# Kernel optimization log

Measured on AMD Instinct MI355X. Metric: run time of the kernel, lower is better.

## Reference

```python
import jax, jax.numpy as jnp
import numpy as np
from jax import lax

N_SERIES = 1024   # embedding rows
B = 1024          # batch (= rows of Y)
T = 512           # n_time
INPUT = 28        # input_size
OUTPUT = 28       # output_size
N_T = 2           # temporal exogenous channels
N_S = 4           # static features
M = 7             # seasonality[0]


def setup_inputs() -> dict:
    key = jax.random.key(0)
    k1, k2, k3, k4, k5 = jax.random.split(key, 5)
    S = jax.random.normal(k1, (B, N_S), jnp.float32)
    # Y must be strictly positive (division + log in normalize)
    Y = jax.random.uniform(k2, (B, T), jnp.float32, 0.5, 1.5)
    X = jax.random.normal(k3, (B, N_T, T), jnp.float32)
    idxs = jax.random.randint(k4, (B,), 0, N_SERIES)
    sample_mask = jnp.ones((B, T), jnp.float32)
    # embedding table, init near 0.5 like the torch module
    embeds_weight = 0.5 + 0.05 * jax.random.normal(k5, (N_SERIES, 1 + 1 + M), jnp.float32)
    return dict(S=S, Y=Y, X=X, idxs=idxs, sample_mask=sample_mask,
                embeds_weight=embeds_weight)


def _levels_seasons(Y, embeds):
    """Single-seasonality (len(seasonality)==1) ES recurrence via lax.scan."""
    lev_sms = jax.nn.sigmoid(embeds[:, 0])      # [B]
    seas_sms = jax.nn.sigmoid(embeds[:, 1])     # [B]
    init_seas = jnp.exp(embeds[:, 2:2 + M])     # [B, M]
    s0 = init_seas[:, 0]                        # [B]
    lev0 = Y[:, 0] / s0                         # levels[0] = Y0 / seas_prod
    # seasonalities1 list = [s0..s_{M-1}, s0]; step t uses index t, so the
    # rolling buffer of the next M seasonal values starts as [s1..s_{M-1}, s0]
    buf0 = jnp.concatenate([init_seas[:, 1:], s0[:, None]], axis=1)  # [B, M]

    def step(carry, y_t):
        lev, buf = carry
        seas_t = buf[:, 0]
        newlev = lev_sms * (y_t / seas_t) + (1.0 - lev_sms) * lev
        newseas = seas_sms * (y_t / newlev) + (1.0 - seas_sms) * seas_t
        buf = jnp.concatenate([buf[:, 1:], newseas[:, None]], axis=1)
        return (newlev, buf), (newlev, newseas)

    (_, _), (levs, seass) = lax.scan(step, (lev0, buf0), Y[:, 1:].T)  # [T-1, B]
    levels = jnp.concatenate([lev0[:, None], levs.T], axis=1)         # [B, T]
    init_list = jnp.concatenate([init_seas, s0[:, None]], axis=1)     # [B, M+1]
    seasonalities = jnp.concatenate([init_list, seass.T], axis=1)     # [B, T+M]
    return levels, seasonalities


def _forward_core(S, Y, X, idxs, sample_mask, embeds_weight):
    embeds = embeds_weight[idxs]                    # embedding lookup [B, 9]
    levels, seasonalities = _levels_seasons(Y, embeds)

    W = T - INPUT - OUTPUT + 1                      # n_windows
    starts = jnp.arange(W)
    idx_in = starts[:, None] + jnp.arange(INPUT)    # [W, INPUT]

    Yw = Y[:, idx_in]                               # [B, W, INPUT]
    lev_end = levels[:, starts + INPUT - 1]         # [B, W] level at window end
    seas_in = seasonalities[:, idx_in]              # [B, W, INPUT]
    insample = jnp.log(Yw / (lev_end[:, :, None] * seas_in))  # [B, W, INPUT]

    # temporal exogenous: X[:, :, start:end+OUTPUT].reshape(B, -1)
    idx_x = starts[:, None] + jnp.arange(INPUT + OUTPUT)       # [W, I+O]
    Xw = X[:, :, idx_x]                              # [B, N_T, W, I+O]
    Xw = jnp.transpose(Xw, (0, 2, 1, 3)).reshape(Y.shape[0], W, N_T * (INPUT + OUTPUT))
    insample = jnp.concatenate([insample, Xw], axis=2)

    # static features
    Sw = jnp.broadcast_to(S[:, None, :], (Y.shape[0], W, N_S))
    insample = jnp.concatenate([insample, Sw], axis=2)          # [B, W, C]
    windows_y_insample = jnp.transpose(insample, (1, 0, 2))     # [W, B, C]

    # outsample (eval mode: raw Y, not normalized)
    idx_out = starts[:, None] + INPUT + jnp.arange(OUTPUT)      # [W, OUTPUT]
    windows_y_outsample = jnp.transpose(Y[:, idx_out], (1, 0, 2))  # [W, B, O]

    # sample_mask unfold(size=OUTPUT, step=1), keep last W windows
    n_unf = T - OUTPUT + 1
    starts_m = jnp.arange(n_unf)[-W:]
    idx_m = starts_m[:, None] + jnp.arange(OUTPUT)
    mask_w = jnp.transpose(sample_mask[:, idx_m], (1, 0, 2))    # [W, B, O]

    return windows_y_insample, windows_y_outsample, levels, seasonalities, mask_w


def reference(S, Y, X, idxs, sample_mask, embeds_weight):
    return _forward_core(S, Y, X, idxs, sample_mask, embeds_weight)
```

## Files before the change

### kernel.cpp

```cpp
#include <hip/hip_runtime.h>

#define BB   1024
#define TT   512
#define NIN  28
#define NOUT 28
#define NS   4
#define MM   7
#define WW   457
#define SLEN 519
#define EMB  9

#define OUT1_SZ (WW * BB * 144)
#define OUT2_SZ (WW * BB * 28)
#define OUT3_SZ (BB * TT)
#define OUT4_SZ (BB * SLEN)

#define CH   32
#define NCH  (TT / CH)

typedef float f4 __attribute__((ext_vector_type(4)));

__device__ __forceinline__ f4 ld4u(const float* p) {
    f4 v;
    __builtin_memcpy(&v, p, sizeof(f4));
    return v;
}

__global__ __launch_bounds__(64) void es_scan(const float* __restrict__ Y,
        const int* __restrict__ idxs, const float* __restrict__ EW,
        float* __restrict__ levels, float* __restrict__ seas) {
    __shared__ float yl[64][CH + 1];
    __shared__ float se[64][CH + 1];
    const int tid = threadIdx.x;
    const int b0  = blockIdx.x << 6;
    const int b   = b0 + tid;

    const float* e = EW + idxs[b] * EMB;
    const float lev_sms  = 1.0f / (1.0f + __expf(-e[0]));
    const float seas_sms = 1.0f / (1.0f + __expf(-e[1]));
    const float a_l = 1.0f - lev_sms;
    const float a_s = 1.0f - seas_sms;

    float buf[MM];
    const float is0 = __expf(e[2]);
    {
        float* srow = seas + b * SLEN;
        srow[0] = is0;
#pragma unroll
        for (int k = 1; k < MM; ++k) {
            float v = __expf(e[2 + k]);
            srow[k] = v;
            buf[k - 1] = v;
        }
        buf[MM - 1] = is0;
    }

    f4 pf[8];
#pragma unroll
    for (int k = 0; k < 8; ++k) {
        int flat = (k << 6) + tid;
        int r = flat >> 3, q = flat & 7;
        pf[k] = *reinterpret_cast<const f4*>(Y + (b0 + r) * TT + (q << 2));
    }

    float lev = 0.0f;

#define ES_STEP(TTI)                                                        \
    {                                                                       \
        float y  = yreg[TTI];                                               \
        float st = buf[0];                                                  \
        lev = lev_sms * __fdividef(y, st) + a_l * lev;                      \
        float ns = seas_sms * __fdividef(y, lev) + a_s * st;                \
        buf[0] = buf[1]; buf[1] = buf[2]; buf[2] = buf[3];                  \
        buf[3] = buf[4]; buf[4] = buf[5]; buf[5] = buf[6];                  \
        buf[6] = ns;                                                        \
        yl[tid][TTI] = lev;                                                 \
        se[tid][TTI] = ns;                                                  \
    }

    for (int c = 0; c < NCH; ++c) {
        __syncthreads();
#pragma unroll
        for (int k = 0; k < 8; ++k) {
            int flat = (k << 6) + tid;
            int r = flat >> 3, q = flat & 7;
            float* dst = &yl[r][q << 2];
            dst[0] = pf[k].x; dst[1] = pf[k].y; dst[2] = pf[k].z; dst[3] = pf[k].w;
        }
        __syncthreads();
        if (c < NCH - 1) {
#pragma unroll
            for (int k = 0; k < 8; ++k) {
                int flat = (k << 6) + tid;
                int r = flat >> 3, q = flat & 7;
                pf[k] = *reinterpret_cast<const f4*>(
                    Y + (b0 + r) * TT + (c + 1) * CH + (q << 2));
            }
        }

        float yreg[CH];
#pragma unroll
        for (int tt = 0; tt < CH; ++tt) yreg[tt] = yl[tid][tt];

        if (c == 0) {
            lev = __fdividef(yreg[0], is0);
            yl[tid][0] = lev;
            se[tid][0] = is0;
#pragma unroll
            for (int tt = 1; tt < CH; ++tt) ES_STEP(tt)
        } else {
#pragma unroll
            for (int tt = 0; tt < CH; ++tt) ES_STEP(tt)
        }
        __syncthreads();

#pragma unroll
        for (int k = 0; k < CH; ++k) {
            int flat = (k << 6) + tid;
            int r    = flat >> 5;
            int col  = flat & 31;
            levels[(b0 + r) * TT   + c * CH + col]      = yl[r][col];
            seas  [(b0 + r) * SLEN + MM + c * CH + col] = se[r][col];
        }
    }
#undef ES_STEP
}

#define PD 129

__global__ __launch_bounds__(256) void k_out1(const float* __restrict__ S,
        const float* __restrict__ Y, const float* __restrict__ X,
        const float* __restrict__ levels, const float* __restrict__ seas,
        f4* __restrict__ out1) {
    __shared__ f4    Xr[4 * 2 * 2 * PD];
    __shared__ f4    LYSr[4 * 2 * PD];
    __shared__ float LL[2][512];
    __shared__ float LYSp[2][520];

    const int tid = threadIdx.x;
    const int b0  = blockIdx.x << 1;

    for (int u = tid; u < 1024; u += 256) {
        int bl = u >> 9, t = u & 511;
        int b  = b0 + bl;
        LL[bl][t]   = __logf(levels[b * TT + t]);
        LYSp[bl][t] = __logf(Y[b * TT + t]) - __logf(seas[b * SLEN + t]);
    }
    __syncthreads();

    for (int u = tid; u < 1024; u += 256) {
        int s = u >> 8, r = u & 255, bl = r >> 7, k = r & 127;
        int base = 4 * k + s;
        f4 v;
        v.x = LYSp[bl][base];     v.y = LYSp[bl][base + 1];
        v.z = LYSp[bl][base + 2]; v.w = LYSp[bl][base + 3];
        LYSr[(s * 2 + bl) * PD + k] = v;
    }
    for (int u = tid; u < 2048; u += 256) {
        int s = u >> 9, r = u & 511, bl = r >> 8, ch = (r >> 7) & 1, k = r & 127;
        int start = 4 * k + s; if (start > 508) start = 508;
        Xr[((s * 2 + bl) * 2 + ch) * PD + k] =
            ld4u(X + (size_t)((b0 + bl) * 2 + ch) * TT + start);
    }
    f4 Sv0 = *reinterpret_cast<const f4*>(S + b0 * NS);
    f4 Sv1 = *reinterpret_cast<const f4*>(S + (b0 + 1) * NS);
    __syncthreads();

    for (int j = tid; j < WW * 72; j += 256) {
        int g   = j / 72;
        int r   = j - g * 72;
        int bl  = (r >= 36) ? 1 : 0;
        int col = r - 36 * bl;
        int s   = g & 3;
        int whi = g >> 2;
        f4 v;
        if (col < 7) {
            f4 t = LYSr[(s * 2 + bl) * PD + whi + col];
            float ll = LL[bl][g + 27];
            v.x = t.x - ll; v.y = t.y - ll; v.z = t.z - ll; v.w = t.w - ll;
        } else if (col < 35) {
            int ch = (col >= 21) ? 1 : 0;
            int jj = col - 7 - 14 * ch;
            v = Xr[((s * 2 + bl) * 2 + ch) * PD + whi + jj];
        } else {
            v = bl ? Sv1 : Sv0;
        }
        __builtin_nontemporal_store(v, &out1[((g << 10) + b0 + bl) * 36 + col]);
    }
}

#define NF2 (WW * BB * 7)

__global__ __launch_bounds__(256) void k_out25(const float* __restrict__ Y,
        const float* __restrict__ mask, f4* __restrict__ out2,
        f4* __restrict__ out5) {
    int i = blockIdx.x * blockDim.x + threadIdx.x;
    const int stride = gridDim.x * blockDim.x;
    for (; i < NF2; i += stride) {
        int wb = i / 7;
        int j  = i - wb * 7;
        int b  = wb & (BB - 1);
        int w  = wb >> 10;
        int base = w + NIN + (j << 2);
        f4 vy = ld4u(Y    + b * TT + base);
        f4 vm = ld4u(mask + b * TT + base);
        __builtin_nontemporal_store(vy, &out2[i]);
        __builtin_nontemporal_store(vm, &out5[i]);
    }
}

extern "C" void kernel_launch(void* const* d_in, const int* in_sizes, int n_in,
                              void* d_out, int out_size, void* d_ws, size_t ws_size,
                              hipStream_t stream) {
    const float* S    = (const float*)d_in[0];
    const float* Y    = (const float*)d_in[1];
    const float* X    = (const float*)d_in[2];
    const int*   idxs = (const int*)d_in[3];
    const float* mask = (const float*)d_in[4];
    const float* EW   = (const float*)d_in[5];

    float* out  = (float*)d_out;
    float* out1 = out;
    float* out2 = out1 + OUT1_SZ;
    float* out3 = out2 + OUT2_SZ;
    float* out4 = out3 + OUT3_SZ;
    float* out5 = out4 + OUT4_SZ;

    es_scan<<<16, 64, 0, stream>>>(Y, idxs, EW, out3, out4);
    k_out1<<<BB / 2, 256, 0, stream>>>(S, Y, X, out3, out4, (f4*)out1);
    k_out25<<<2048, 256, 0, stream>>>(Y, mask, (f4*)out2, (f4*)out5);
}
```

Baseline: 130.0 us.

## Fuse ES scan with out2/out5 copy kernel and split out1 across more blocks

The serial ES scan (16 blocks) now shares one launch with the out2/out5 gather copy, so the copy blocks fill the GPU while the scan runs instead of waiting behind it. The scan blocks grow to 256 threads, with only 64 doing the recurrence and all helping with loads and stores. k_out1 is split four ways along the window dimension (2048 blocks) and reads unrotated shared arrays with scalar LDS loads instead of the pre-rotated f4 layout. Each k_out1 block still recomputes the logs for its full rows, which repeats transcendental work four times.

```diff
diff --git a/kernel.cpp b/kernel.cpp
--- a/kernel.cpp
+++ b/kernel.cpp
@@ -17,6 +17,7 @@
 
 #define CH   32
 #define NCH  (TT / CH)
+#define NF2  (WW * BB * 7)
 
 typedef float f4 __attribute__((ext_vector_type(4)));
 
@@ -26,44 +27,49 @@
     return v;
 }
 
-__global__ __launch_bounds__(64) void es_scan(const float* __restrict__ Y,
-        const int* __restrict__ idxs, const float* __restrict__ EW,
-        float* __restrict__ levels, float* __restrict__ seas) {
+__global__ __launch_bounds__(256, 8) void k_scan_out25(
+        const float* __restrict__ Y, const int* __restrict__ idxs,
+        const float* __restrict__ EW, const float* __restrict__ mask,
+        float* __restrict__ levels, float* __restrict__ seas,
+        f4* __restrict__ out2, f4* __restrict__ out5) {
     __shared__ float yl[64][CH + 1];
     __shared__ float se[64][CH + 1];
+
     const int tid = threadIdx.x;
-    const int b0  = blockIdx.x << 6;
-    const int b   = b0 + tid;
-
-    const float* e = EW + idxs[b] * EMB;
-    const float lev_sms  = 1.0f / (1.0f + __expf(-e[0]));
-    const float seas_sms = 1.0f / (1.0f + __expf(-e[1]));
-    const float a_l = 1.0f - lev_sms;
-    const float a_s = 1.0f - seas_sms;
-
-    float buf[MM];
-    const float is0 = __expf(e[2]);
-    {
-        float* srow = seas + b * SLEN;
-        srow[0] = is0;
-#pragma unroll
-        for (int k = 1; k < MM; ++k) {
-            float v = __expf(e[2 + k]);
-            srow[k] = v;
-            buf[k - 1] = v;
-        }
-        buf[MM - 1] = is0;
-    }
-
-    f4 pf[8];
-#pragma unroll
-    for (int k = 0; k < 8; ++k) {
-        int flat = (k << 6) + tid;
-        int r = flat >> 3, q = flat & 7;
-        pf[k] = *reinterpret_cast<const f4*>(Y + (b0 + r) * TT + (q << 2));
-    }
-
-    float lev = 0.0f;
+
+    if (blockIdx.x < 16) {
+        const int b0 = blockIdx.x << 6;
+        const int bs = b0 + (tid & 63);
+
+        const float* e = EW + idxs[bs] * EMB;
+        const float lev_sms  = 1.0f / (1.0f + __expf(-e[0]));
+        const float seas_sms = 1.0f / (1.0f + __expf(-e[1]));
+        const float a_l = 1.0f - lev_sms;
+        const float a_s = 1.0f - seas_sms;
+
+        float buf[MM];
+        const float is0 = __expf(e[2]);
+        {
+            float* srow = seas + bs * SLEN;
+            if (tid < 64) srow[0] = is0;
+#pragma unroll
+            for (int k = 1; k < MM; ++k) {
+                float v = __expf(e[2 + k]);
+                if (tid < 64) srow[k] = v;
+                buf[k - 1] = v;
+            }
+            buf[MM - 1] = is0;
+        }
+
+        f4 pf[2];
+#pragma unroll
+        for (int k = 0; k < 2; ++k) {
+            int flat = (k << 8) + tid;
+            int r = flat >> 3, q = flat & 7;
+            pf[k] = *reinterpret_cast<const f4*>(Y + (b0 + r) * TT + (q << 2));
+        }
+
+        float lev = 0.0f;
 
 #define ES_STEP(TTI)                                                        \
     {                                                                       \
@@ -78,134 +84,124 @@
         se[tid][TTI] = ns;                                                  \
     }
 
-    for (int c = 0; c < NCH; ++c) {
-        __syncthreads();
-#pragma unroll
-        for (int k = 0; k < 8; ++k) {
-            int flat = (k << 6) + tid;
-            int r = flat >> 3, q = flat & 7;
-            float* dst = &yl[r][q << 2];
-            dst[0] = pf[k].x; dst[1] = pf[k].y; dst[2] = pf[k].z; dst[3] = pf[k].w;
-        }
-        __syncthreads();
-        if (c < NCH - 1) {
+        for (int c = 0; c < NCH; ++c) {
+            __syncthreads();
+#pragma unroll
+            for (int k = 0; k < 2; ++k) {
+                int flat = (k << 8) + tid;
+                int r = flat >> 3, q = flat & 7;
+                float* dst = &yl[r][q << 2];
+                dst[0] = pf[k].x; dst[1] = pf[k].y;
+                dst[2] = pf[k].z; dst[3] = pf[k].w;
+            }
+            __syncthreads();
+            if (c < NCH - 1) {
+#pragma unroll
+                for (int k = 0; k < 2; ++k) {
+                    int flat = (k << 8) + tid;
+                    int r = flat >> 3, q = flat & 7;
+                    pf[k] = *reinterpret_cast<const f4*>(
+                        Y + (b0 + r) * TT + (c + 1) * CH + (q << 2));
+                }
+            }
+
+            if (tid < 64) {
+                float yreg[CH];
+#pragma unroll
+                for (int tt = 0; tt < CH; ++tt) yreg[tt] = yl[tid][tt];
+
+                if (c == 0) {
+                    lev = __fdividef(yreg[0], is0);
+                    yl[tid][0] = lev;
+                    se[tid][0] = is0;
+#pragma unroll
+                    for (int tt = 1; tt < CH; ++tt) ES_STEP(tt)
+                } else {
+#pragma unroll
+                    for (int tt = 0; tt < CH; ++tt) ES_STEP(tt)
+                }
+            }
+            __syncthreads();
+
 #pragma unroll
             for (int k = 0; k < 8; ++k) {
-                int flat = (k << 6) + tid;
-                int r = flat >> 3, q = flat & 7;
-                pf[k] = *reinterpret_cast<const f4*>(
-                    Y + (b0 + r) * TT + (c + 1) * CH + (q << 2));
-            }
-        }
-
-        float yreg[CH];
-#pragma unroll
-        for (int tt = 0; tt < CH; ++tt) yreg[tt] = yl[tid][tt];
-
-        if (c == 0) {
-            lev = __fdividef(yreg[0], is0);
-            yl[tid][0] = lev;
-            se[tid][0] = is0;
-#pragma unroll
-            for (int tt = 1; tt < CH; ++tt) ES_STEP(tt)
-        } else {
-#pragma unroll
-            for (int tt = 0; tt < CH; ++tt) ES_STEP(tt)
-        }
-        __syncthreads();
-
-#pragma unroll
-        for (int k = 0; k < CH; ++k) {
-            int flat = (k << 6) + tid;
-            int r    = flat >> 5;
-            int col  = flat & 31;
-            levels[(b0 + r) * TT   + c * CH + col]      = yl[r][col];
-            seas  [(b0 + r) * SLEN + MM + c * CH + col] = se[r][col];
-        }
-    }
+                int flat = (k << 8) + tid;
+                int r    = flat >> 5;
+                int col  = flat & 31;
+                levels[(b0 + r) * TT   + c * CH + col]      = yl[r][col];
+                seas  [(b0 + r) * SLEN + MM + c * CH + col] = se[r][col];
+            }
+        }
 #undef ES_STEP
-}
-
-#define PD 129
-
-__global__ __launch_bounds__(256) void k_out1(const float* __restrict__ S,
+    } else {
+        const int id = blockIdx.x - 16;
+        for (int i = (id << 8) + tid; i < NF2; i += 2048 * 256) {
+            int wb = i / 7;
+            int j  = i - wb * 7;
+            int b  = wb & (BB - 1);
+            int w  = wb >> 10;
+            int base = w + NIN + (j << 2);
+            f4 vy = ld4u(Y    + b * TT + base);
+            f4 vm = ld4u(mask + b * TT + base);
+            __builtin_nontemporal_store(vy, &out2[i]);
+            __builtin_nontemporal_store(vm, &out5[i]);
+        }
+    }
+}
+
+#define QW 115
+
+__global__ __launch_bounds__(256, 8) void k_out1(const float* __restrict__ S,
         const float* __restrict__ Y, const float* __restrict__ X,
         const float* __restrict__ levels, const float* __restrict__ seas,
         f4* __restrict__ out1) {
-    __shared__ f4    Xr[4 * 2 * 2 * PD];
-    __shared__ f4    LYSr[4 * 2 * PD];
-    __shared__ float LL[2][512];
-    __shared__ float LYSp[2][520];
+    __shared__ float Xs[2][2][TT];
+    __shared__ float LYSp[2][TT];
+    __shared__ float LLs[2][TT];
 
     const int tid = threadIdx.x;
-    const int b0  = blockIdx.x << 1;
-
+    const int p   = blockIdx.x >> 2;
+    const int qt  = blockIdx.x & 3;
+    const int b0  = p << 1;
+    const int g0  = qt * QW;
+    const int NW  = (qt == 3) ? (WW - 3 * QW) : QW;
+
+    for (int u = tid; u < 2048; u += 256) {
+        int bl = u >> 10, ch = (u >> 9) & 1, t = u & 511;
+        Xs[bl][ch][t] = X[(size_t)((b0 + bl) * 2 + ch) * TT + t];
+    }
     for (int u = tid; u < 1024; u += 256) {
         int bl = u >> 9, t = u & 511;
         int b  = b0 + bl;
-        LL[bl][t]   = __logf(levels[b * TT + t]);
+        LLs[bl][t]  = __logf(levels[b * TT + t]);
         LYSp[bl][t] = __logf(Y[b * TT + t]) - __logf(seas[b * SLEN + t]);
-    }
-    __syncthreads();
-
-    for (int u = tid; u < 1024; u += 256) {
-        int s = u >> 8, r = u & 255, bl = r >> 7, k = r & 127;
-        int base = 4 * k + s;
-        f4 v;
-        v.x = LYSp[bl][base];     v.y = LYSp[bl][base + 1];
-        v.z = LYSp[bl][base + 2]; v.w = LYSp[bl][base + 3];
-        LYSr[(s * 2 + bl) * PD + k] = v;
-    }
-    for (int u = tid; u < 2048; u += 256) {
-        int s = u >> 9, r = u & 511, bl = r >> 8, ch = (r >> 7) & 1, k = r & 127;
-        int start = 4 * k + s; if (start > 508) start = 508;
-        Xr[((s * 2 + bl) * 2 + ch) * PD + k] =
-            ld4u(X + (size_t)((b0 + bl) * 2 + ch) * TT + start);
     }
     f4 Sv0 = *reinterpret_cast<const f4*>(S + b0 * NS);
     f4 Sv1 = *reinterpret_cast<const f4*>(S + (b0 + 1) * NS);
     __syncthreads();
 
-    for (int j = tid; j < WW * 72; j += 256) {
-        int g   = j / 72;
-        int r   = j - g * 72;
-        int bl  = (r >= 36) ? 1 : 0;
-        int col = r - 36 * bl;
-        int s   = g & 3;
-        int whi = g >> 2;
+    const int NJ = NW * 72;
+    for (int jj = tid; jj < NJ; jj += 256) {
+        int grel = jj / 72;
+        int r    = jj - grel * 72;
+        int g    = g0 + grel;
+        int bl   = (r >= 36) ? 1 : 0;
+        int col  = r - 36 * bl;
         f4 v;
         if (col < 7) {
-            f4 t = LYSr[(s * 2 + bl) * PD + whi + col];
-            float ll = LL[bl][g + 27];
-            v.x = t.x - ll; v.y = t.y - ll; v.z = t.z - ll; v.w = t.w - ll;
+            int t    = g + (col << 2);
+            float ll = LLs[bl][g + 27];
+            v.x = LYSp[bl][t]     - ll; v.y = LYSp[bl][t + 1] - ll;
+            v.z = LYSp[bl][t + 2] - ll; v.w = LYSp[bl][t + 3] - ll;
         } else if (col < 35) {
             int ch = (col >= 21) ? 1 : 0;
-            int jj = col - 7 - 14 * ch;
-            v = Xr[((s * 2 + bl) * 2 + ch) * PD + whi + jj];
+            int t  = g + ((col - 7 - 14 * ch) << 2);
+            v.x = Xs[bl][ch][t];     v.y = Xs[bl][ch][t + 1];
+            v.z = Xs[bl][ch][t + 2]; v.w = Xs[bl][ch][t + 3];
         } else {
             v = bl ? Sv1 : Sv0;
         }
         __builtin_nontemporal_store(v, &out1[((g << 10) + b0 + bl) * 36 + col]);
-    }
-}
-
-#define NF2 (WW * BB * 7)
-
-__global__ __launch_bounds__(256) void k_out25(const float* __restrict__ Y,
-        const float* __restrict__ mask, f4* __restrict__ out2,
-        f4* __restrict__ out5) {
-    int i = blockIdx.x * blockDim.x + threadIdx.x;
-    const int stride = gridDim.x * blockDim.x;
-    for (; i < NF2; i += stride) {
-        int wb = i / 7;
-        int j  = i - wb * 7;
-        int b  = wb & (BB - 1);
-        int w  = wb >> 10;
-        int base = w + NIN + (j << 2);
-        f4 vy = ld4u(Y    + b * TT + base);
-        f4 vm = ld4u(mask + b * TT + base);
-        __builtin_nontemporal_store(vy, &out2[i]);
-        __builtin_nontemporal_store(vm, &out5[i]);
     }
 }
 
@@ -226,7 +222,7 @@
     float* out4 = out3 + OUT3_SZ;
     float* out5 = out4 + OUT4_SZ;
 
-    es_scan<<<16, 64, 0, stream>>>(Y, idxs, EW, out3, out4);
-    k_out1<<<BB / 2, 256, 0, stream>>>(S, Y, X, out3, out4, (f4*)out1);
-    k_out25<<<2048, 256, 0, stream>>>(Y, mask, (f4*)out2, (f4*)out5);
-}
+    k_scan_out25<<<2064, 256, 0, stream>>>(Y, idxs, EW, mask, out3, out4,
+                                           (f4*)out2, (f4*)out5);
+    k_out1<<<2048, 256, 0, stream>>>(S, Y, X, out3, out4, (f4*)out1);
+}
```

Measured after the change: 159.0 us. 22.3% more time.

## Split out1 kernel per batch pair into two halves with branchless strided store loop

Applied to the files above, without the earlier changes.

The windowed-feature kernel now runs 1024 blocks of 512 threads, with each block handling half of the windows for a pair of batch rows. Staging reads global memory directly into a compact shared layout, with no intermediate transpose pass and only one barrier. Each thread keeps a fixed output column and walks windows with precomputed shared-memory strides, so the per-element division and branching is gone. X and S columns subtract a zero log-level, so every column takes the same code path. In exchange there is more index bookkeeping and the log work is duplicated across the two halves.

```diff
diff --git a/kernel.cpp b/kernel.cpp
--- a/kernel.cpp
+++ b/kernel.cpp
@@ -17,6 +17,7 @@
 
 #define CH   32
 #define NCH  (TT / CH)
+#define NF2  (WW * BB * 7)
 
 typedef float f4 __attribute__((ext_vector_type(4)));
 
@@ -126,70 +127,93 @@
 #undef ES_STEP
 }
 
-#define PD 129
-
-__global__ __launch_bounds__(256) void k_out1(const float* __restrict__ S,
-        const float* __restrict__ Y, const float* __restrict__ X,
+#define SBLK 420
+#define D0q  (3 * SBLK + 1)
+#define D1q  (2 - SBLK)
+#define OST  (7 * 1024 * 36)
+
+__global__ __launch_bounds__(512) void k_out1(const float* __restrict__ Y,
+        const float* __restrict__ X, const float* __restrict__ S,
         const float* __restrict__ levels, const float* __restrict__ seas,
         f4* __restrict__ out1) {
-    __shared__ f4    Xr[4 * 2 * 2 * PD];
-    __shared__ f4    LYSr[4 * 2 * PD];
-    __shared__ float LL[2][512];
-    __shared__ float LYSp[2][520];
+    __shared__ f4    R[4 * SBLK + 3];
+    __shared__ float LLf[1026];
 
     const int tid = threadIdx.x;
-    const int b0  = blockIdx.x << 1;
-
-    for (int u = tid; u < 1024; u += 256) {
-        int bl = u >> 9, t = u & 511;
-        int b  = b0 + bl;
-        LL[bl][t]   = __logf(levels[b * TT + t]);
-        LYSp[bl][t] = __logf(Y[b * TT + t]) - __logf(seas[b * SLEN + t]);
-    }
+    const int p   = blockIdx.x >> 1;
+    const int h   = blockIdx.x & 1;
+    const int b0  = p << 1;
+    const int g0  = h ? 229 : 0;
+    const int NW  = h ? 228 : 229;
+
+    {
+        int s = tid >> 7, bl = (tid >> 6) & 1, k = tid & 63;
+        int base = g0 + 4 * k + s;
+        f4 yv = ld4u(Y    + (b0 + bl) * TT   + base);
+        f4 sv = ld4u(seas + (b0 + bl) * SLEN + base);
+        f4 v;
+        v.x = __logf(yv.x) - __logf(sv.x);
+        v.y = __logf(yv.y) - __logf(sv.y);
+        v.z = __logf(yv.z) - __logf(sv.z);
+        v.w = __logf(yv.w) - __logf(sv.w);
+        R[s * SBLK + bl * 64 + k] = v;
+    }
+    for (int u = tid; u < 1152; u += 512) {
+        int s = u / 288, rem = u - s * 288;
+        int blc = rem / 72, k = rem - blc * 72;
+        int base = g0 + 4 * k + s;
+        if (base > 508) base = 508;
+        R[s * SBLK + 128 + blc * 72 + k] =
+            ld4u(X + (size_t)((b0 + (blc >> 1)) * 2 + (blc & 1)) * TT + base);
+    }
+    for (int u = tid; u < 1024; u += 512)
+        LLf[u] = __logf(levels[(b0 + (u >> 9)) * TT + (u & 511)]);
+    if (tid < 2) R[4 * SBLK + tid] = *reinterpret_cast<const f4*>(S + (b0 + tid) * NS);
+    if (tid == 2) { f4 z; z.x = z.y = z.z = z.w = 0.0f; R[4 * SBLK + 2] = z; }
+    if (tid == 3) LLf[1024] = 0.0f;
     __syncthreads();
 
-    for (int u = tid; u < 1024; u += 256) {
-        int s = u >> 8, r = u & 255, bl = r >> 7, k = r & 127;
-        int base = 4 * k + s;
-        f4 v;
-        v.x = LYSp[bl][base];     v.y = LYSp[bl][base + 1];
-        v.z = LYSp[bl][base + 2]; v.w = LYSp[bl][base + 3];
-        LYSr[(s * 2 + bl) * PD + k] = v;
-    }
-    for (int u = tid; u < 2048; u += 256) {
-        int s = u >> 9, r = u & 511, bl = r >> 8, ch = (r >> 7) & 1, k = r & 127;
-        int start = 4 * k + s; if (start > 508) start = 508;
-        Xr[((s * 2 + bl) * 2 + ch) * PD + k] =
-            ld4u(X + (size_t)((b0 + bl) * 2 + ch) * TT + start);
-    }
-    f4 Sv0 = *reinterpret_cast<const f4*>(S + b0 * NS);
-    f4 Sv1 = *reinterpret_cast<const f4*>(S + (b0 + 1) * NS);
-    __syncthreads();
-
-    for (int j = tid; j < WW * 72; j += 256) {
-        int g   = j / 72;
-        int r   = j - g * 72;
-        int bl  = (r >= 36) ? 1 : 0;
-        int col = r - 36 * bl;
-        int s   = g & 3;
-        int whi = g >> 2;
-        f4 v;
+    if (tid < 504) {
+        const int go  = tid / 72;
+        const int r   = tid - go * 72;
+        const int bl  = (r >= 36) ? 1 : 0;
+        const int col = r - 36 * bl;
+        const int s0  = go & 3;
+        const int wh0 = go >> 2;
+
+        int qa, la, ls, mv;
         if (col < 7) {
-            f4 t = LYSr[(s * 2 + bl) * PD + whi + col];
-            float ll = LL[bl][g + 27];
-            v.x = t.x - ll; v.y = t.y - ll; v.z = t.z - ll; v.w = t.w - ll;
+            qa = s0 * SBLK + bl * 64 + wh0 + col;
+            la = bl * 512 + g0 + go + 27;
+            ls = 7;  mv = 1;
         } else if (col < 35) {
             int ch = (col >= 21) ? 1 : 0;
             int jj = col - 7 - 14 * ch;
-            v = Xr[((s * 2 + bl) * 2 + ch) * PD + whi + jj];
+            qa = s0 * SBLK + 128 + (bl * 2 + ch) * 72 + wh0 + jj;
+            la = 1024;  ls = 0;  mv = 1;
         } else {
-            v = bl ? Sv1 : Sv0;
-        }
-        __builtin_nontemporal_store(v, &out1[((g << 10) + b0 + bl) * 36 + col]);
-    }
-}
-
-#define NF2 (WW * BB * 7)
+            qa = 4 * SBLK + bl;
+            la = 1024;  ls = 0;  mv = 0;
+        }
+        const int dA = mv ? ((((s0    ) & 3) == 0) ? D0q : D1q) : 0;
+        const int dB = mv ? ((((s0 + 3) & 3) == 0) ? D0q : D1q) : 0;
+        const int dC = mv ? ((((s0 + 2) & 3) == 0) ? D0q : D1q) : 0;
+        const int dD = mv ? ((((s0 + 1) & 3) == 0) ? D0q : D1q) : 0;
+        int off = (((g0 + go) << 10) + b0 + bl) * 36 + col;
+
+#define STEP1(DQ)                                                           \
+        { f4 q = R[qa]; float l = LLf[la];                                  \
+          f4 v; v.x = q.x - l; v.y = q.y - l; v.z = q.z - l; v.w = q.w - l; \
+          __builtin_nontemporal_store(v, out1 + off);                       \
+          qa += DQ; la += ls; off += OST; }
+
+        for (int it = 0; it < 8; ++it) {
+            STEP1(dA) STEP1(dB) STEP1(dC) STEP1(dD)
+        }
+        if (go + 224 < NW) STEP1(dA)
+#undef STEP1
+    }
+}
 
 __global__ __launch_bounds__(256) void k_out25(const float* __restrict__ Y,
         const float* __restrict__ mask, f4* __restrict__ out2,
@@ -227,6 +251,6 @@
     float* out5 = out4 + OUT4_SZ;
 
     es_scan<<<16, 64, 0, stream>>>(Y, idxs, EW, out3, out4);
-    k_out1<<<BB / 2, 256, 0, stream>>>(S, Y, X, out3, out4, (f4*)out1);
+    k_out1<<<1024, 512, 0, stream>>>(Y, X, S, out3, out4, (f4*)out1);
     k_out25<<<2048, 256, 0, stream>>>(Y, mask, (f4*)out2, (f4*)out5);
 }
```

After: 127.8 us. About the same (-1.7%).

## Restructure window-output kernel into two time halves with register-prefetched staging

Applied to the files above, without the earlier changes.

The out1 kernel now uses 512 threads and splits the window range into two halves of about 229 windows. Each half stages only its slice of log-levels, log(Y/seas), X and S in a small shared buffer, and loads for the second half are issued into registers while the first half is being stored. Each thread writes a fixed output column across many windows with strided nontemporal stores, replacing the old per-element division and modulo indexing. The goal is less shared memory, better occupancy and overlap of global loads with the large output write, at the cost of more complex index math and heavier per-thread register use.

```diff
diff --git a/kernel.cpp b/kernel.cpp
--- a/kernel.cpp
+++ b/kernel.cpp
@@ -3,7 +3,6 @@
 #define BB   1024
 #define TT   512
 #define NIN  28
-#define NOUT 28
 #define NS   4
 #define MM   7
 #define WW   457
@@ -17,6 +16,7 @@
 
 #define CH   32
 #define NCH  (TT / CH)
+#define NF2  (WW * BB * 7)
 
 typedef float f4 __attribute__((ext_vector_type(4)));
 
@@ -126,70 +126,124 @@
 #undef ES_STEP
 }
 
-#define PD 129
-
-__global__ __launch_bounds__(256) void k_out1(const float* __restrict__ S,
-        const float* __restrict__ Y, const float* __restrict__ X,
+#define LYSo 0
+#define LYSs 273
+#define XSo  546
+#define XSs  293
+#define LLo  1718
+#define LLs  237
+#define SSo  2192
+#define ZRo  2200
+#define ULEN 2201
+#define OST  (7 * 1024 * 36)
+
+__device__ __forceinline__ void tload(int i, int g0, int b0,
+        const float* __restrict__ Y, const float* __restrict__ seas,
+        const float* __restrict__ X, const float* __restrict__ levels,
+        f4& a, f4& b) {
+    if (i < 128) {
+        int bl = i >> 6, k = i & 63, t = g0 + (k << 2);
+        a = ld4u(Y    + (b0 + bl) * TT   + t);
+        b = ld4u(seas + (b0 + bl) * SLEN + t);
+    } else if (i < 412) {
+        int j = i - 128, blc = j / 71, k = j - blc * 71;
+        int t = g0 + (k << 2); if (t > 508) t = 508;
+        a = ld4u(X + (size_t)((b0 + (blc >> 1)) * 2 + (blc & 1)) * TT + t);
+    } else if (i < 528) {
+        int j = i - 412, bl = j / 58, k = j - bl * 58;
+        a = ld4u(levels + (b0 + bl) * TT + g0 + 24 + (k << 2));
+    }
+}
+
+__device__ __forceinline__ void twrite(int i, int g0, float* U, f4 a, f4 b) {
+    if (i < 128) {
+        int bl = i >> 6, k = i & 63, base = LYSo + bl * LYSs + (k << 2);
+        U[base + 0] = __logf(a.x) - __logf(b.x);
+        U[base + 1] = __logf(a.y) - __logf(b.y);
+        U[base + 2] = __logf(a.z) - __logf(b.z);
+        U[base + 3] = __logf(a.w) - __logf(b.w);
+    } else if (i < 412) {
+        int j = i - 128, blc = j / 71, k = j - blc * 71;
+        int wb = (k << 2); if (g0 + wb > 508) wb = 508 - g0;
+        int base = XSo + blc * XSs + wb;
+        U[base + 0] = a.x; U[base + 1] = a.y;
+        U[base + 2] = a.z; U[base + 3] = a.w;
+    } else if (i < 528) {
+        int j = i - 412, bl = j / 58, k = j - bl * 58;
+        int base = LLo + bl * LLs + (k << 2);
+        U[base + 0] = __logf(a.x); U[base + 1] = __logf(a.y);
+        U[base + 2] = __logf(a.z); U[base + 3] = __logf(a.w);
+    }
+}
+
+__device__ __forceinline__ void tstore(int tid, int g0, int NW, int b0,
+        const float* U, f4* __restrict__ out1) {
+    if (tid >= 504) return;
+    int go  = tid / 72;
+    int r   = tid - go * 72;
+    int bl  = (r >= 36) ? 1 : 0;
+    int col = r - 36 * bl;
+    int pa, la, dp, dl;
+    if (col < 7) {
+        pa = LYSo + bl * LYSs + go + (col << 2);
+        la = LLo  + bl * LLs  + go + 3;
+        dp = 7; dl = 7;
+    } else if (col < 35) {
+        int ch = (col >= 21) ? 1 : 0;
+        int jj = col - 7 - 14 * ch;
+        pa = XSo + ((bl << 1) | ch) * XSs + go + (jj << 2);
+        la = ZRo; dp = 7; dl = 0;
+    } else {
+        pa = SSo + (bl << 2);
+        la = ZRo; dp = 0; dl = 0;
+    }
+    int off = (((g0 + go) << 10) + b0 + bl) * 36 + col;
+#define ST1 { float l = U[la]; f4 v;                                        \
+    v.x = U[pa] - l; v.y = U[pa + 1] - l;                                   \
+    v.z = U[pa + 2] - l; v.w = U[pa + 3] - l;                               \
+    __builtin_nontemporal_store(v, out1 + off);                             \
+    pa += dp; la += dl; off += OST; }
+#pragma unroll 4
+    for (int t = 0; t < 32; ++t) ST1
+    if (go + 224 < NW) ST1
+#undef ST1
+}
+
+__global__ __launch_bounds__(512) void k_out1(const float* __restrict__ Y,
+        const float* __restrict__ X, const float* __restrict__ S,
         const float* __restrict__ levels, const float* __restrict__ seas,
         f4* __restrict__ out1) {
-    __shared__ f4    Xr[4 * 2 * 2 * PD];
-    __shared__ f4    LYSr[4 * 2 * PD];
-    __shared__ float LL[2][512];
-    __shared__ float LYSp[2][520];
-
+    __shared__ float U[ULEN];
     const int tid = threadIdx.x;
-    const int b0  = blockIdx.x << 1;
-
-    for (int u = tid; u < 1024; u += 256) {
-        int bl = u >> 9, t = u & 511;
-        int b  = b0 + bl;
-        LL[bl][t]   = __logf(levels[b * TT + t]);
-        LYSp[bl][t] = __logf(Y[b * TT + t]) - __logf(seas[b * SLEN + t]);
-    }
+    const int b0  = (int)blockIdx.x << 1;
+
+    f4 a, b, e, eb, a2, b2, e2, eb2, sv;
+
+    tload(tid, 0, b0, Y, seas, X, levels, a, b);
+    if (tid < 16) tload(512 + tid, 0, b0, Y, seas, X, levels, e, eb);
+    if (tid < 2)  sv = *reinterpret_cast<const f4*>(S + ((b0 + tid) << 2));
+
+    twrite(tid, 0, U, a, b);
+    if (tid < 16) twrite(512 + tid, 0, U, e, eb);
+    if (tid < 2) {
+        int base = SSo + (tid << 2);
+        U[base] = sv.x; U[base + 1] = sv.y; U[base + 2] = sv.z; U[base + 3] = sv.w;
+    }
+    if (tid == 2) U[ZRo] = 0.0f;
     __syncthreads();
 
-    for (int u = tid; u < 1024; u += 256) {
-        int s = u >> 8, r = u & 255, bl = r >> 7, k = r & 127;
-        int base = 4 * k + s;
-        f4 v;
-        v.x = LYSp[bl][base];     v.y = LYSp[bl][base + 1];
-        v.z = LYSp[bl][base + 2]; v.w = LYSp[bl][base + 3];
-        LYSr[(s * 2 + bl) * PD + k] = v;
-    }
-    for (int u = tid; u < 2048; u += 256) {
-        int s = u >> 9, r = u & 511, bl = r >> 8, ch = (r >> 7) & 1, k = r & 127;
-        int start = 4 * k + s; if (start > 508) start = 508;
-        Xr[((s * 2 + bl) * 2 + ch) * PD + k] =
-            ld4u(X + (size_t)((b0 + bl) * 2 + ch) * TT + start);
-    }
-    f4 Sv0 = *reinterpret_cast<const f4*>(S + b0 * NS);
-    f4 Sv1 = *reinterpret_cast<const f4*>(S + (b0 + 1) * NS);
+    tload(tid, 229, b0, Y, seas, X, levels, a2, b2);
+    if (tid < 16) tload(512 + tid, 229, b0, Y, seas, X, levels, e2, eb2);
+
+    tstore(tid, 0, 229, b0, U, out1);
     __syncthreads();
 
-    for (int j = tid; j < WW * 72; j += 256) {
-        int g   = j / 72;
-        int r   = j - g * 72;
-        int bl  = (r >= 36) ? 1 : 0;
-        int col = r - 36 * bl;
-        int s   = g & 3;
-        int whi = g >> 2;
-        f4 v;
-        if (col < 7) {
-            f4 t = LYSr[(s * 2 + bl) * PD + whi + col];
-            float ll = LL[bl][g + 27];
-            v.x = t.x - ll; v.y = t.y - ll; v.z = t.z - ll; v.w = t.w - ll;
-        } else if (col < 35) {
-            int ch = (col >= 21) ? 1 : 0;
-            int jj = col - 7 - 14 * ch;
-            v = Xr[((s * 2 + bl) * 2 + ch) * PD + whi + jj];
-        } else {
-            v = bl ? Sv1 : Sv0;
-        }
-        __builtin_nontemporal_store(v, &out1[((g << 10) + b0 + bl) * 36 + col]);
-    }
-}
-
-#define NF2 (WW * BB * 7)
+    twrite(tid, 229, U, a2, b2);
+    if (tid < 16) twrite(512 + tid, 229, U, e2, eb2);
+    __syncthreads();
+
+    tstore(tid, 229, 228, b0, U, out1);
+}
 
 __global__ __launch_bounds__(256) void k_out25(const float* __restrict__ Y,
         const float* __restrict__ mask, f4* __restrict__ out2,
@@ -227,6 +281,6 @@
     float* out5 = out4 + OUT4_SZ;
 
     es_scan<<<16, 64, 0, stream>>>(Y, idxs, EW, out3, out4);
-    k_out1<<<BB / 2, 256, 0, stream>>>(S, Y, X, out3, out4, (f4*)out1);
+    k_out1<<<512, 512, 0, stream>>>(Y, X, S, out3, out4, (f4*)out1);
     k_out25<<<2048, 256, 0, stream>>>(Y, mask, (f4*)out2, (f4*)out5);
 }
```

New measurement: 126.3 us. -2.8%, faster.
